# Performance work log

Hardware: AMD Instinct MI355X
Metric: run time of the kernel (lower is better)

Reference implementation:

```python
import jax, jax.numpy as jnp
import numpy as np

N_NODES = 50000
N_EDGES = 800000
F_IN = 128


def _sage_conv(x, src, dst, W_l, b_l, W_r, n_nodes):
    # PyG SAGEConv (mean aggr, normalize=False, root_weight=True):
    #   out_i = W_l @ mean_{j in N(i)} x_j + b_l + W_r @ x_i
    msg = x[src]  # [E, F] gather
    agg = jax.ops.segment_sum(msg, dst, num_segments=n_nodes)  # [N, F]
    cnt = jax.ops.segment_sum(jnp.ones((src.shape[0],), x.dtype), dst,
                              num_segments=n_nodes)  # [N]
    mean = agg / jnp.maximum(cnt, 1.0)[:, None]
    return mean @ W_l.T + b_l + x @ W_r.T


def setup_inputs() -> dict:
    key = jax.random.key(0)
    ks = jax.random.split(key, 16)
    inp = {}
    inp["x"] = jax.random.normal(ks[0], (N_NODES, F_IN), dtype=jnp.float32)
    inp["edge_index"] = jax.random.randint(ks[1], (2, N_EDGES), 0, N_NODES, dtype=jnp.int64)
    inp["reg_id"] = jax.random.randint(ks[2], (N_NODES,), 0, 22, dtype=jnp.int64)
    inp["dep_id"] = jax.random.randint(ks[3], (N_NODES,), 0, 96, dtype=jnp.int64)
    # learned parameters (kaiming-ish small random)
    inp["W_feat"] = jax.random.normal(ks[4], (32, F_IN), dtype=jnp.float32) * (1.0 / np.sqrt(F_IN))
    inp["b_feat"] = jnp.zeros((32,), dtype=jnp.float32)
    inp["reg_emb"] = jax.random.normal(ks[5], (22, 16), dtype=jnp.float32)
    inp["dep_emb"] = jax.random.normal(ks[6], (96, 16), dtype=jnp.float32)
    inp["W1_l"] = jax.random.normal(ks[7], (16, 64), dtype=jnp.float32) * 0.125
    inp["b1_l"] = jnp.zeros((16,), dtype=jnp.float32)
    inp["W1_r"] = jax.random.normal(ks[8], (16, 64), dtype=jnp.float32) * 0.125
    inp["W2_l"] = jax.random.normal(ks[9], (32, 16), dtype=jnp.float32) * 0.25
    inp["b2_l"] = jnp.zeros((32,), dtype=jnp.float32)
    inp["W2_r"] = jax.random.normal(ks[10], (32, 16), dtype=jnp.float32) * 0.25
    inp["W_lin"] = jax.random.normal(ks[11], (1, 32), dtype=jnp.float32) * 0.1767767
    inp["b_lin"] = jnp.zeros((1,), dtype=jnp.float32)
    return inp


def reference(x, edge_index, reg_id, dep_id, W_feat, b_feat, reg_emb, dep_emb,
              W1_l, b1_l, W1_r, W2_l, b2_l, W2_r, W_lin, b_lin):
    src, dst = edge_index[0], edge_index[1]
    reg_fm = reg_emb[reg_id]            # [N, 16]
    dep_fm = dep_emb[dep_id]            # [N, 16]
    h = x @ W_feat.T + b_feat           # [N, 32]
    h = jnp.concatenate([h, reg_fm, dep_fm], axis=1)  # [N, 64]
    h = jax.nn.relu(_sage_conv(h, src, dst, W1_l, b1_l, W1_r, N_NODES))  # [N, 16]
    h = jax.nn.relu(_sage_conv(h, src, dst, W2_l, b2_l, W2_r, N_NODES))  # [N, 32]
    return h @ W_lin.T + b_lin          # [N, 1]
```

## Files before the change

kernel.cpp:

```cpp
#include <hip/hip_runtime.h>

#define N_NODES 50000
#define N_EDGES 800000
#define HB 128
#define CHUNK (N_EDGES / HB)
#define CNTW ((N_NODES + 3) / 4)
#define NODE1_BLOCKS ((N_NODES + 63) / 64)
#define SCAN_BLK 256
#define SCAN_NBLK ((N_NODES + SCAN_BLK - 1) / SCAN_BLK)

__device__ __forceinline__ unsigned short f2bf(float f) {
    unsigned int b = __float_as_uint(f);
    b += 0x7fffu + ((b >> 16) & 1u);
    return (unsigned short)(b >> 16);
}

__global__ __launch_bounds__(256) void node1_hist_kernel(
    const float* __restrict__ x, const int* __restrict__ reg_id,
    const int* __restrict__ dep_id,
    const float* __restrict__ W_feat, const float* __restrict__ b_feat,
    const float* __restrict__ reg_emb, const float* __restrict__ dep_emb,
    const float* __restrict__ W1_l, const float* __restrict__ W1_r,
    const int* __restrict__ ei,
    unsigned short* __restrict__ p1bf, float* __restrict__ r1,
    unsigned int* __restrict__ part, unsigned char* __restrict__ lrank)
{
    __shared__ union U {
        struct N1 { float sx[64 * 132]; float sh[64 * 68]; } n1;
        unsigned int cnt[CNTW];
    } u;
    const int tid = threadIdx.x;

    if (blockIdx.x >= NODE1_BLOCKS) {
        const int g  = blockIdx.x - NODE1_BLOCKS;
        const int e0 = g * CHUNK;
        for (int i = tid; i < CNTW; i += 256) u.cnt[i] = 0u;
        __syncthreads();
        for (int i = tid; i < CHUNK; i += 256) {
            int d = ei[N_EDGES + e0 + i];
            unsigned sh_ = (unsigned)(d & 3) * 8u;
            unsigned old = atomicAdd(&u.cnt[d >> 2], 1u << sh_);
            lrank[e0 + i] = (unsigned char)((old >> sh_) & 0xffu);
        }
        __syncthreads();
        for (int i = tid; i < CNTW; i += 256)
            part[g * CNTW + i] = u.cnt[i];
        return;
    }

    const int node0 = blockIdx.x * 64;
    for (int i = tid; i < 64 * 32; i += 256) {
        int row = i >> 5, c4 = i & 31;
        float4 v = make_float4(0.f, 0.f, 0.f, 0.f);
        int n = node0 + row;
        if (n < N_NODES) v = *(const float4*)&x[n * 128 + c4 * 4];
        *(float4*)&u.n1.sx[row * 132 + c4 * 4] = v;
    }
    for (int i = tid; i < 64 * 16; i += 256) {
        int r = i >> 4, f = i & 15;
        int n = node0 + r;
        if (n < N_NODES) {
            u.n1.sh[r * 68 + 32 + f] = reg_emb[reg_id[n] * 16 + f];
            u.n1.sh[r * 68 + 48 + f] = dep_emb[dep_id[n] * 16 + f];
        }
    }
    __syncthreads();

    const int nl = tid & 63;
    const int j0 = __builtin_amdgcn_readfirstlane((tid >> 6) * 8);

    {
        float acc[8];
        #pragma unroll
        for (int jj = 0; jj < 8; ++jj) acc[jj] = b_feat[j0 + jj];
        #pragma unroll 4
        for (int k = 0; k < 128; k += 4) {
            float4 xv = *(const float4*)&u.n1.sx[nl * 132 + k];
            #pragma unroll
            for (int jj = 0; jj < 8; ++jj) {
                const float* wr = &W_feat[(j0 + jj) * 128 + k];
                acc[jj] += xv.x * wr[0] + xv.y * wr[1] + xv.z * wr[2] + xv.w * wr[3];
            }
        }
        #pragma unroll
        for (int jj = 0; jj < 8; ++jj) u.n1.sh[nl * 68 + j0 + jj] = acc[jj];
    }
    __syncthreads();

    {
        const float* Wbase = (j0 < 16) ? (W1_l + j0 * 64) : (W1_r + (j0 - 16) * 64);
        float acc[8];
        #pragma unroll
        for (int jj = 0; jj < 8; ++jj) acc[jj] = 0.f;
        #pragma unroll 4
        for (int k = 0; k < 64; k += 4) {
            float4 hv = *(const float4*)&u.n1.sh[nl * 68 + k];
            #pragma unroll
            for (int jj = 0; jj < 8; ++jj) {
                const float* wr = &Wbase[jj * 64 + k];
                acc[jj] += hv.x * wr[0] + hv.y * wr[1] + hv.z * wr[2] + hv.w * wr[3];
            }
        }
        int n = node0 + nl;
        if (n < N_NODES) {
            if (j0 < 16) {
                uint4 q;
                q.x = ((unsigned)f2bf(acc[1]) << 16) | f2bf(acc[0]);
                q.y = ((unsigned)f2bf(acc[3]) << 16) | f2bf(acc[2]);
                q.z = ((unsigned)f2bf(acc[5]) << 16) | f2bf(acc[4]);
                q.w = ((unsigned)f2bf(acc[7]) << 16) | f2bf(acc[6]);
                *(uint4*)&p1bf[n * 16 + j0] = q;
            } else {
                float* outp = r1 + n * 16 + (j0 - 16);
                *(float4*)outp       = make_float4(acc[0], acc[1], acc[2], acc[3]);
                *(float4*)(outp + 4) = make_float4(acc[4], acc[5], acc[6], acc[7]);
            }
        }
    }
}

__global__ __launch_bounds__(256) void bpscan_kernel(
    const unsigned int* __restrict__ part, unsigned char* __restrict__ bp,
    int* __restrict__ rowp1, int* __restrict__ parts)
{
    __shared__ int buf[2][256];
    int t = threadIdx.x;
    int n = blockIdx.x * 256 + t;
    int deg = 0;
    if (n < N_NODES) {
        int w = n >> 2;
        unsigned sh_ = (unsigned)(n & 3) * 8u;
        int s = 0;
        #pragma unroll 16
        for (int b = 0; b < HB; ++b) {
            bp[(size_t)b * N_NODES + n] = (unsigned char)s;
            s += (int)((part[b * CNTW + w] >> sh_) & 0xffu);
        }
        deg = s;
    }
    buf[0][t] = deg;
    __syncthreads();
    int cur = 0;
    for (int off = 1; off < 256; off <<= 1) {
        int nv = buf[cur][t] + ((t >= off) ? buf[cur][t - off] : 0);
        buf[cur ^ 1][t] = nv;
        cur ^= 1;
        __syncthreads();
    }
    int incl = buf[cur][t];
    if (n < N_NODES) rowp1[n] = incl - deg;
    if (t == 255) parts[blockIdx.x] = incl;
}

__global__ __launch_bounds__(256) void scanparts_kernel(
    const int* __restrict__ parts, int* __restrict__ poff)
{
    __shared__ int buf[2][256];
    int t = threadIdx.x;
    int pv = (t < SCAN_NBLK) ? parts[t] : 0;
    buf[0][t] = pv;
    __syncthreads();
    int cur = 0;
    for (int off = 1; off < 256; off <<= 1) {
        int nv = buf[cur][t] + ((t >= off) ? buf[cur][t - off] : 0);
        buf[cur ^ 1][t] = nv;
        cur ^= 1;
        __syncthreads();
    }
    if (t < SCAN_NBLK) poff[t] = buf[cur][t] - pv;
}

__global__ __launch_bounds__(256) void fill_kernel(
    const int* __restrict__ ei, const unsigned char* __restrict__ lrank,
    const int* __restrict__ rowp1, const int* __restrict__ poff,
    const unsigned char* __restrict__ bp, int* __restrict__ csrc)
{
    int t4 = (blockIdx.x * 256 + threadIdx.x) * 4;
    if (t4 >= N_EDGES) return;
    uint4 sv = *(const uint4*)&ei[t4];
    uint4 dv = *(const uint4*)&ei[N_EDGES + t4];
    unsigned lr4 = *(const unsigned*)&lrank[t4];

    #pragma unroll
    for (int j = 0; j < 4; ++j) {
        int d = (j == 0) ? (int)dv.x : (j == 1) ? (int)dv.y
              : (j == 2) ? (int)dv.z : (int)dv.w;
        int s = (j == 0) ? (int)sv.x : (j == 1) ? (int)sv.y
              : (j == 2) ? (int)sv.z : (int)sv.w;
        int g = (t4 + j) / CHUNK;
        int pos = rowp1[d] + poff[d >> 8] + (int)bp[(size_t)g * N_NODES + d]
                + (int)((lr4 >> (8 * j)) & 0xffu);
        csrc[pos] = s;
    }
}

__global__ __launch_bounds__(256) void gather1_kernel(
    const int* __restrict__ rowp1, const int* __restrict__ poff,
    const int* __restrict__ csrc,
    const unsigned short* __restrict__ p1bf, const float* __restrict__ r1,
    const float* __restrict__ b1_l, unsigned short* __restrict__ h1bf)
{
    int n = (blockIdx.x * 256 + threadIdx.x) >> 6;
    int lane = threadIdx.x & 63;
    int slot = lane >> 2, f4 = lane & 3;
    int start = rowp1[n] + poff[n >> 8];
    int end = (n + 1 < N_NODES) ? rowp1[n + 1] + poff[(n + 1) >> 8] : N_EDGES;

    float4 acc = make_float4(0.f, 0.f, 0.f, 0.f);
    for (int eb = start; eb < end; eb += 16) {
        int e = eb + slot;
        if (e < end) {
            uint2 v = *(const uint2*)&p1bf[csrc[e] * 16 + f4 * 4];
            acc.x += __uint_as_float(v.x << 16);
            acc.y += __uint_as_float(v.x & 0xffff0000u);
            acc.z += __uint_as_float(v.y << 16);
            acc.w += __uint_as_float(v.y & 0xffff0000u);
        }
    }
    #pragma unroll
    for (int off = 4; off <= 32; off <<= 1) {
        acc.x += __shfl_xor(acc.x, off, 64);
        acc.y += __shfl_xor(acc.y, off, 64);
        acc.z += __shfl_xor(acc.z, off, 64);
        acc.w += __shfl_xor(acc.w, off, 64);
    }
    if (slot == 0) {
        float inv = 1.0f / fmaxf((float)(end - start), 1.0f);
        float4 rv = *(const float4*)&r1[n * 16 + f4 * 4];
        float4 bv = *(const float4*)&b1_l[f4 * 4];
        float ox = fmaxf(acc.x * inv + bv.x + rv.x, 0.f);
        float oy = fmaxf(acc.y * inv + bv.y + rv.y, 0.f);
        float oz = fmaxf(acc.z * inv + bv.z + rv.z, 0.f);
        float ow = fmaxf(acc.w * inv + bv.w + rv.w, 0.f);
        uint2 w;
        w.x = ((unsigned)f2bf(oy) << 16) | f2bf(ox);
        w.y = ((unsigned)f2bf(ow) << 16) | f2bf(oz);
        *(uint2*)&h1bf[n * 16 + f4 * 4] = w;
    }
}

__global__ __launch_bounds__(256) void gather2_kernel(
    const int* __restrict__ rowp1, const int* __restrict__ poff,
    const int* __restrict__ csrc, const unsigned short* __restrict__ h1bf,
    const float* __restrict__ W2_l, const float* __restrict__ b2_l,
    const float* __restrict__ W2_r, const float* __restrict__ W_lin,
    const float* __restrict__ b_lin, float* __restrict__ out)
{
    int n = (blockIdx.x * 256 + threadIdx.x) >> 6;
    int lane = threadIdx.x & 63;
    int slot = lane >> 2, f4 = lane & 3;
    int start = rowp1[n] + poff[n >> 8];
    int end = (n + 1 < N_NODES) ? rowp1[n + 1] + poff[(n + 1) >> 8] : N_EDGES;

    float4 acc = make_float4(0.f, 0.f, 0.f, 0.f);
    for (int eb = start; eb < end; eb += 16) {
        int e = eb + slot;
        if (e < end) {
            uint2 v = *(const uint2*)&h1bf[csrc[e] * 16 + f4 * 4];
            acc.x += __uint_as_float(v.x << 16);
            acc.y += __uint_as_float(v.x & 0xffff0000u);
            acc.z += __uint_as_float(v.y << 16);
            acc.w += __uint_as_float(v.y & 0xffff0000u);
        }
    }
    #pragma unroll
    for (int off = 4; off <= 32; off <<= 1) {
        acc.x += __shfl_xor(acc.x, off, 64);
        acc.y += __shfl_xor(acc.y, off, 64);
        acc.z += __shfl_xor(acc.z, off, 64);
        acc.w += __shfl_xor(acc.w, off, 64);
    }
    float inv = 1.0f / fmaxf((float)(end - start), 1.0f);
    float4 m2 = make_float4(acc.x * inv, acc.y * inv, acc.z * inv, acc.w * inv);
    uint2 hv = *(const uint2*)&h1bf[n * 16 + f4 * 4];
    float hn0 = __uint_as_float(hv.x << 16);
    float hn1 = __uint_as_float(hv.x & 0xffff0000u);
    float hn2 = __uint_as_float(hv.y << 16);
    float hn3 = __uint_as_float(hv.y & 0xffff0000u);

    int j0 = slot * 2;
    float4 wl0 = *(const float4*)&W2_l[j0 * 16 + f4 * 4];
    float4 wl1 = *(const float4*)&W2_l[(j0 + 1) * 16 + f4 * 4];
    float4 wr0 = *(const float4*)&W2_r[j0 * 16 + f4 * 4];
    float4 wr1 = *(const float4*)&W2_r[(j0 + 1) * 16 + f4 * 4];

    float pa = m2.x * wl0.x + m2.y * wl0.y + m2.z * wl0.z + m2.w * wl0.w
             + hn0 * wr0.x + hn1 * wr0.y + hn2 * wr0.z + hn3 * wr0.w;
    float pb = m2.x * wl1.x + m2.y * wl1.y + m2.z * wl1.z + m2.w * wl1.w
             + hn0 * wr1.x + hn1 * wr1.y + hn2 * wr1.z + hn3 * wr1.w;
    pa += __shfl_xor(pa, 1, 64); pa += __shfl_xor(pa, 2, 64);
    pb += __shfl_xor(pb, 1, 64); pb += __shfl_xor(pb, 2, 64);

    float h2a = fmaxf(pa + b2_l[j0], 0.f);
    float h2b = fmaxf(pb + b2_l[j0 + 1], 0.f);
    float w = h2a * W_lin[j0] + h2b * W_lin[j0 + 1];
    #pragma unroll
    for (int off = 4; off <= 32; off <<= 1) w += __shfl_xor(w, off, 64);
    if (lane == 0) out[n] = w + b_lin[0];
}

extern "C" void kernel_launch(void* const* d_in, const int* in_sizes, int n_in,
                              void* d_out, int out_size, void* d_ws, size_t ws_size,
                              hipStream_t stream) {
    const float* x       = (const float*)d_in[0];
    const int*   ei      = (const int*)  d_in[1];
    const int*   reg_id  = (const int*)  d_in[2];
    const int*   dep_id  = (const int*)  d_in[3];
    const float* W_feat  = (const float*)d_in[4];
    const float* b_feat  = (const float*)d_in[5];
    const float* reg_emb = (const float*)d_in[6];
    const float* dep_emb = (const float*)d_in[7];
    const float* W1_l    = (const float*)d_in[8];
    const float* b1_l    = (const float*)d_in[9];
    const float* W1_r    = (const float*)d_in[10];
    const float* W2_l    = (const float*)d_in[11];
    const float* b2_l    = (const float*)d_in[12];
    const float* W2_r    = (const float*)d_in[13];
    const float* W_lin   = (const float*)d_in[14];
    const float* b_lin   = (const float*)d_in[15];
    float* out = (float*)d_out;
    float* ws  = (float*)d_ws;

    const int N = N_NODES;
    float* r1 = ws;
    unsigned int* part = (unsigned int*)(ws + 16 * N);
    int* csrc  = (int*)(part + HB * CNTW);
    int* rowp1 = csrc + N_EDGES;
    int* parts = rowp1 + N;
    int* poff  = parts + 256;
    unsigned short* p1bf = (unsigned short*)(poff + 256);
    unsigned short* h1bf = p1bf + 16 * N;
    unsigned char* lrank = (unsigned char*)(h1bf + 16 * N);
    unsigned char* bp    = lrank + N_EDGES;

    node1_hist_kernel<<<NODE1_BLOCKS + HB, 256, 0, stream>>>(
        x, reg_id, dep_id, W_feat, b_feat, reg_emb, dep_emb, W1_l, W1_r,
        ei, p1bf, r1, part, lrank);

    bpscan_kernel<<<SCAN_NBLK, 256, 0, stream>>>(part, bp, rowp1, parts);

    scanparts_kernel<<<1, 256, 0, stream>>>(parts, poff);

    fill_kernel<<<(N_EDGES / 4 + 255) / 256, 256, 0, stream>>>(
        ei, lrank, rowp1, poff, bp, csrc);

    gather1_kernel<<<(N * 64) / 256, 256, 0, stream>>>(
        rowp1, poff, csrc, p1bf, r1, b1_l, h1bf);

    gather2_kernel<<<(N * 64) / 256, 256, 0, stream>>>(
        rowp1, poff, csrc, h1bf, W2_l, b2_l, W2_r, W_lin, b_lin, out);
}
```

Baseline: 102.8 us.

## Read x directly from global in node1 and schedule histogram blocks first

```diff
diff --git a/kernel.cpp b/kernel.cpp
--- a/kernel.cpp
+++ b/kernel.cpp
@@ -26,13 +26,13 @@
     unsigned int* __restrict__ part, unsigned char* __restrict__ lrank)
 {
     __shared__ union U {
-        struct N1 { float sx[64 * 132]; float sh[64 * 68]; } n1;
+        float sh[64 * 68];
         unsigned int cnt[CNTW];
     } u;
     const int tid = threadIdx.x;
 
-    if (blockIdx.x >= NODE1_BLOCKS) {
-        const int g  = blockIdx.x - NODE1_BLOCKS;
+    if (blockIdx.x < HB) {
+        const int g  = blockIdx.x;
         const int e0 = g * CHUNK;
         for (int i = tid; i < CNTW; i += 256) u.cnt[i] = 0u;
         __syncthreads();
@@ -48,34 +48,28 @@
         return;
     }
 
-    const int node0 = blockIdx.x * 64;
-    for (int i = tid; i < 64 * 32; i += 256) {
-        int row = i >> 5, c4 = i & 31;
-        float4 v = make_float4(0.f, 0.f, 0.f, 0.f);
-        int n = node0 + row;
-        if (n < N_NODES) v = *(const float4*)&x[n * 128 + c4 * 4];
-        *(float4*)&u.n1.sx[row * 132 + c4 * 4] = v;
-    }
+    const int node0 = (blockIdx.x - HB) * 64;
+    const int nl = tid & 63;
+    const int j0 = __builtin_amdgcn_readfirstlane((tid >> 6) * 8);
+    const int n  = node0 + nl;
+
     for (int i = tid; i < 64 * 16; i += 256) {
         int r = i >> 4, f = i & 15;
-        int n = node0 + r;
-        if (n < N_NODES) {
-            u.n1.sh[r * 68 + 32 + f] = reg_emb[reg_id[n] * 16 + f];
-            u.n1.sh[r * 68 + 48 + f] = dep_emb[dep_id[n] * 16 + f];
-        }
-    }
-    __syncthreads();
-
-    const int nl = tid & 63;
-    const int j0 = __builtin_amdgcn_readfirstlane((tid >> 6) * 8);
-
-    {
+        int nn = node0 + r;
+        if (nn < N_NODES) {
+            u.sh[r * 68 + 32 + f] = reg_emb[reg_id[nn] * 16 + f];
+            u.sh[r * 68 + 48 + f] = dep_emb[dep_id[nn] * 16 + f];
+        }
+    }
+
+    if (n < N_NODES) {
+        const float* xrow = &x[(size_t)n * 128];
         float acc[8];
         #pragma unroll
         for (int jj = 0; jj < 8; ++jj) acc[jj] = b_feat[j0 + jj];
         #pragma unroll 4
         for (int k = 0; k < 128; k += 4) {
-            float4 xv = *(const float4*)&u.n1.sx[nl * 132 + k];
+            float4 xv = *(const float4*)&xrow[k];
             #pragma unroll
             for (int jj = 0; jj < 8; ++jj) {
                 const float* wr = &W_feat[(j0 + jj) * 128 + k];
@@ -83,38 +77,35 @@
             }
         }
         #pragma unroll
-        for (int jj = 0; jj < 8; ++jj) u.n1.sh[nl * 68 + j0 + jj] = acc[jj];
+        for (int jj = 0; jj < 8; ++jj) u.sh[nl * 68 + j0 + jj] = acc[jj];
     }
     __syncthreads();
 
-    {
+    if (n < N_NODES) {
         const float* Wbase = (j0 < 16) ? (W1_l + j0 * 64) : (W1_r + (j0 - 16) * 64);
         float acc[8];
         #pragma unroll
         for (int jj = 0; jj < 8; ++jj) acc[jj] = 0.f;
         #pragma unroll 4
         for (int k = 0; k < 64; k += 4) {
-            float4 hv = *(const float4*)&u.n1.sh[nl * 68 + k];
+            float4 hv = *(const float4*)&u.sh[nl * 68 + k];
             #pragma unroll
             for (int jj = 0; jj < 8; ++jj) {
                 const float* wr = &Wbase[jj * 64 + k];
                 acc[jj] += hv.x * wr[0] + hv.y * wr[1] + hv.z * wr[2] + hv.w * wr[3];
             }
         }
-        int n = node0 + nl;
-        if (n < N_NODES) {
-            if (j0 < 16) {
-                uint4 q;
-                q.x = ((unsigned)f2bf(acc[1]) << 16) | f2bf(acc[0]);
-                q.y = ((unsigned)f2bf(acc[3]) << 16) | f2bf(acc[2]);
-                q.z = ((unsigned)f2bf(acc[5]) << 16) | f2bf(acc[4]);
-                q.w = ((unsigned)f2bf(acc[7]) << 16) | f2bf(acc[6]);
-                *(uint4*)&p1bf[n * 16 + j0] = q;
-            } else {
-                float* outp = r1 + n * 16 + (j0 - 16);
-                *(float4*)outp       = make_float4(acc[0], acc[1], acc[2], acc[3]);
-                *(float4*)(outp + 4) = make_float4(acc[4], acc[5], acc[6], acc[7]);
-            }
+        if (j0 < 16) {
+            uint4 q;
+            q.x = ((unsigned)f2bf(acc[1]) << 16) | f2bf(acc[0]);
+            q.y = ((unsigned)f2bf(acc[3]) << 16) | f2bf(acc[2]);
+            q.z = ((unsigned)f2bf(acc[5]) << 16) | f2bf(acc[4]);
+            q.w = ((unsigned)f2bf(acc[7]) << 16) | f2bf(acc[6]);
+            *(uint4*)&p1bf[n * 16 + j0] = q;
+        } else {
+            float* outp = r1 + n * 16 + (j0 - 16);
+            *(float4*)outp       = make_float4(acc[0], acc[1], acc[2], acc[3]);
+            *(float4*)(outp + 4) = make_float4(acc[4], acc[5], acc[6], acc[7]);
         }
     }
 }
```

After: 105.9 us. +3.0%, slower.
